# Kernel tuning notes

Measured on AMD Instinct MI355X. Metric: run time of the kernel, lower is better.

## Reference

```python
import jax, jax.numpy as jnp
import numpy as np

B, T, A = 4096, 32, 3
HID, D, N, K = 1024, 128, 16, 4096
FLAT = T * A            # 96
LAT = N * D             # 2048
COMMIT = 0.25


def setup_inputs() -> dict:
    key = jax.random.key(0)
    ks = jax.random.split(key, 14)
    s = 0.02
    return {
        "actions": jax.random.normal(ks[0], (B, T, A), jnp.float32),
        # encoder: FLAT -> HID -> HID -> N*D
        "e_w1": jax.random.normal(ks[1], (FLAT, HID), jnp.float32) * s,
        "e_b1": jnp.zeros((HID,), jnp.float32),
        "e_w2": jax.random.normal(ks[2], (HID, HID), jnp.float32) * s,
        "e_b2": jnp.zeros((HID,), jnp.float32),
        "e_w3": jax.random.normal(ks[3], (HID, LAT), jnp.float32) * s,
        "e_b3": jnp.zeros((LAT,), jnp.float32),
        # codebook init: uniform(-1/K, 1/K) as in torch init
        "codebook": jax.random.uniform(ks[4], (K, D), jnp.float32, -1.0 / K, 1.0 / K),
        # decoder: N*D -> HID -> HID -> FLAT
        "d_w1": jax.random.normal(ks[5], (LAT, HID), jnp.float32) * s,
        "d_b1": jnp.zeros((HID,), jnp.float32),
        "d_w2": jax.random.normal(ks[6], (HID, HID), jnp.float32) * s,
        "d_b2": jnp.zeros((HID,), jnp.float32),
        "d_w3": jax.random.normal(ks[7], (HID, FLAT), jnp.float32) * s,
        "d_b3": jnp.zeros((FLAT,), jnp.float32),
    }


def reference(actions, e_w1, e_b1, e_w2, e_b2, e_w3, e_b3, codebook,
              d_w1, d_b1, d_w2, d_b2, d_w3, d_b3):
    sg = jax.lax.stop_gradient
    b = actions.shape[0]
    # encode: [B, T*A] -> [B, N, D]
    flat = actions.reshape(b, FLAT)
    h = jax.nn.silu(flat @ e_w1 + e_b1)
    h = jax.nn.silu(h @ e_w2 + e_b2)
    latents = (h @ e_w3 + e_b3).reshape(b, N, D)
    # nearest-code search: [B*N, K] squared distances
    fl = latents.reshape(b * N, D)
    dist = (fl * fl).sum(1, keepdims=True) + (codebook * codebook).sum(1)[None, :] - 2.0 * (fl @ codebook.T)
    indices = jnp.argmin(dist, axis=1).reshape(b, N)
    quantized = codebook[indices]                      # [B, N, D]
    codebook_loss = jnp.mean((quantized - sg(latents)) ** 2)
    commitment_loss = jnp.mean((latents - sg(quantized)) ** 2)
    vq_loss = codebook_loss + COMMIT * commitment_loss
    q_st = latents + sg(quantized - latents)           # straight-through
    # decode
    g = jax.nn.silu(q_st.reshape(b, LAT) @ d_w1 + d_b1)
    g = jax.nn.silu(g @ d_w2 + d_b2)
    recon = (g @ d_w3 + d_b3).reshape(b, T, A)
    recon_loss = jnp.mean((recon - actions) ** 2)
    loss = recon_loss + vq_loss
    return recon, indices, vq_loss, recon_loss, loss
```

## Files before the change

kernel.cpp:

```cpp
#include <hip/hip_runtime.h>
#include <hip/hip_bf16.h>

#define DD 128

typedef float f2v __attribute__((ext_vector_type(2)));

__global__ void plant_diag(float val, float* out) {
    if (threadIdx.x == 0 && blockIdx.x == 0) out[0] = val;
}

__global__ void zero_acc(double* acc) {
    if (threadIdx.x == 0 && blockIdx.x == 0) { acc[0] = 0.0; acc[1] = 0.0; }
}

__device__ __forceinline__ float silu_np(float x) {
    float e = (float)exp(-(double)x);
    float u = 1.0f + e;
    float v = 1.0f / u;
    return x * v;
}

template <bool SILU>
__global__ __launch_bounds__(256) void gemm_db(const float* __restrict__ A,
                                               const float* __restrict__ W,
                                               const float* __restrict__ bias,
                                               float* __restrict__ C,
                                               int M, int N, int K) {
    __shared__ __align__(16) float As[128][36];
    __shared__ __align__(16) float Ws[32][68];
    const int t = threadIdx.x;
    const int tx = t & 15, ty = t >> 4;
    const int bm = blockIdx.y * 128, bn = blockIdx.x * 64;

    float acc[8][4];
#pragma unroll
    for (int i = 0; i < 8; ++i)
#pragma unroll
        for (int j = 0; j < 4; ++j) acc[i][j] = 0.0f;

    const int nPanels = (K + 31) / 32;
    float ra[16], rw[8];

    {
        const int k0 = 0;
#pragma unroll
        for (int it = 0; it < 16; ++it) {
            int e = t + 256 * it;
            int m = e >> 5, kk = e & 31;
            int mm = bm + m; if (mm >= M) mm = M - 1;
            int kc = k0 + kk;
            ra[it] = (kc < K) ? A[(size_t)mm * K + kc] : 0.0f;
        }
#pragma unroll
        for (int it = 0; it < 8; ++it) {
            int e = t + 256 * it;
            int r = e >> 6, c = e & 63;
            int n = bn + c;
            int kr = k0 + r;
            rw[it] = (kr < K && n < N) ? W[(size_t)kr * N + n] : 0.0f;
        }
    }

    for (int p = 0; p < nPanels; ++p) {
        __syncthreads();
#pragma unroll
        for (int it = 0; it < 16; ++it) {
            int e = t + 256 * it;
            As[e >> 5][e & 31] = ra[it];
        }
#pragma unroll
        for (int it = 0; it < 8; ++it) {
            int e = t + 256 * it;
            Ws[e >> 6][e & 63] = rw[it];
        }
        __syncthreads();

        if (p + 1 < nPanels) {
            const int k0 = (p + 1) * 32;
#pragma unroll
            for (int it = 0; it < 16; ++it) {
                int e = t + 256 * it;
                int m = e >> 5, kk = e & 31;
                int mm = bm + m; if (mm >= M) mm = M - 1;
                int kc = k0 + kk;
                ra[it] = (kc < K) ? A[(size_t)mm * K + kc] : 0.0f;
            }
#pragma unroll
            for (int it = 0; it < 8; ++it) {
                int e = t + 256 * it;
                int r = e >> 6, c = e & 63;
                int n = bn + c;
                int kr = k0 + r;
                rw[it] = (kr < K && n < N) ? W[(size_t)kr * N + n] : 0.0f;
            }
        }

#pragma unroll
        for (int kq = 0; kq < 8; ++kq) {
            float4 a4[8], w4[4];
#pragma unroll
            for (int i = 0; i < 8; ++i)
                a4[i] = *(const float4*)&As[ty + 16 * i][4 * kq];
#pragma unroll
            for (int q = 0; q < 4; ++q)
                w4[q] = *(const float4*)&Ws[4 * kq + q][4 * tx];
#pragma unroll
            for (int q = 0; q < 4; ++q) {
                const float wv[4] = {w4[q].x, w4[q].y, w4[q].z, w4[q].w};
#pragma unroll
                for (int i = 0; i < 8; ++i) {
                    const float av = ((const float*)&a4[i])[q];
#pragma unroll
                    for (int j = 0; j < 4; ++j)
                        acc[i][j] = fmaf(av, wv[j], acc[i][j]);
                }
            }
        }
    }

#pragma unroll
    for (int i = 0; i < 8; ++i) {
        int m = bm + ty + 16 * i;
#pragma unroll
        for (int j = 0; j < 4; ++j) {
            int n = bn + 4 * tx + j;
            if (m < M && n < N) {
                float x = acc[i][j] + bias[n];
                if (SILU) x = silu_np(x);
                C[(size_t)m * N + n] = x;
            }
        }
    }
}

template <bool SILU>
__global__ __launch_bounds__(256) void gemm64(const float* __restrict__ A,
                                              const float* __restrict__ W,
                                              const float* __restrict__ bias,
                                              float* __restrict__ C,
                                              int M, int N, int K) {
    __shared__ __align__(16) float As[64][36];
    __shared__ __align__(16) float Ws[32][68];
    const int t = threadIdx.x;
    const int tx = t & 15, ty = t >> 4;
    const int bm = blockIdx.y * 64, bn = blockIdx.x * 64;

    float acc[4][4];
#pragma unroll
    for (int i = 0; i < 4; ++i)
#pragma unroll
        for (int j = 0; j < 4; ++j) acc[i][j] = 0.0f;

    const int nPanels = (K + 31) / 32;
    float ra[8], rw[8];

    {
        const int k0 = 0;
#pragma unroll
        for (int it = 0; it < 8; ++it) {
            int e = t + 256 * it;
            int m = e >> 5, kk = e & 31;
            int mm = bm + m; if (mm >= M) mm = M - 1;
            int kc = k0 + kk;
            ra[it] = (kc < K) ? A[(size_t)mm * K + kc] : 0.0f;
            int r = e >> 6, c = e & 63;
            int n = bn + c;
            int kr = k0 + r;
            rw[it] = (kr < K && n < N) ? W[(size_t)kr * N + n] : 0.0f;
        }
    }

    for (int p = 0; p < nPanels; ++p) {
        __syncthreads();
#pragma unroll
        for (int it = 0; it < 8; ++it) {
            int e = t + 256 * it;
            As[e >> 5][e & 31] = ra[it];
            Ws[e >> 6][e & 63] = rw[it];
        }
        __syncthreads();

        if (p + 1 < nPanels) {
            const int k0 = (p + 1) * 32;
#pragma unroll
            for (int it = 0; it < 8; ++it) {
                int e = t + 256 * it;
                int m = e >> 5, kk = e & 31;
                int mm = bm + m; if (mm >= M) mm = M - 1;
                int kc = k0 + kk;
                ra[it] = (kc < K) ? A[(size_t)mm * K + kc] : 0.0f;
                int r = e >> 6, c = e & 63;
                int n = bn + c;
                int kr = k0 + r;
                rw[it] = (kr < K && n < N) ? W[(size_t)kr * N + n] : 0.0f;
            }
        }

#pragma unroll
        for (int kq = 0; kq < 8; ++kq) {
            float4 a4[4], w4[4];
#pragma unroll
            for (int i = 0; i < 4; ++i)
                a4[i] = *(const float4*)&As[4 * ty + i][4 * kq];
#pragma unroll
            for (int q = 0; q < 4; ++q)
                w4[q] = *(const float4*)&Ws[4 * kq + q][4 * tx];
#pragma unroll
            for (int q = 0; q < 4; ++q) {
                const float wv[4] = {w4[q].x, w4[q].y, w4[q].z, w4[q].w};
                const float av[4] = {((const float*)&a4[0])[q], ((const float*)&a4[1])[q],
                                     ((const float*)&a4[2])[q], ((const float*)&a4[3])[q]};
#pragma unroll
                for (int i = 0; i < 4; ++i)
#pragma unroll
                    for (int j = 0; j < 4; ++j)
                        acc[i][j] = fmaf(av[i], wv[j], acc[i][j]);
            }
        }
    }

#pragma unroll
    for (int i = 0; i < 4; ++i) {
        int m = bm + 4 * ty + i;
#pragma unroll
        for (int j = 0; j < 4; ++j) {
            int n = bn + 4 * tx + j;
            if (m < M && n < N) {
                float x = acc[i][j] + bias[n];
                if (SILU) x = silu_np(x);
                C[(size_t)m * N + n] = x;
            }
        }
    }
}

__device__ __forceinline__ float pairwise128_sq(const float* __restrict__ x, int stride) {
    float r0 = x[0*stride]*x[0*stride], r1 = x[1*stride]*x[1*stride],
          r2 = x[2*stride]*x[2*stride], r3 = x[3*stride]*x[3*stride],
          r4 = x[4*stride]*x[4*stride], r5 = x[5*stride]*x[5*stride],
          r6 = x[6*stride]*x[6*stride], r7 = x[7*stride]*x[7*stride];
    for (int i = 8; i < 128; i += 8) {
        r0 += x[(i+0)*stride]*x[(i+0)*stride];
        r1 += x[(i+1)*stride]*x[(i+1)*stride];
        r2 += x[(i+2)*stride]*x[(i+2)*stride];
        r3 += x[(i+3)*stride]*x[(i+3)*stride];
        r4 += x[(i+4)*stride]*x[(i+4)*stride];
        r5 += x[(i+5)*stride]*x[(i+5)*stride];
        r6 += x[(i+6)*stride]*x[(i+6)*stride];
        r7 += x[(i+7)*stride]*x[(i+7)*stride];
    }
    return ((r0 + r1) + (r2 + r3)) + ((r4 + r5) + (r6 + r7));
}

__global__ void code_t2(const float* __restrict__ cb, float* __restrict__ t2, int K) {
    int k = blockIdx.x * 256 + threadIdx.x;
    if (k >= K) return;
    t2[k] = pairwise128_sq(cb + (size_t)k * DD, 1);
}

__global__ void cb_pack(const float* __restrict__ cb, float* __restrict__ cbP, int total) {
    int gid = blockIdx.x * 256 + threadIdx.x;
    if (gid >= total) return;
    int pair = gid >> 8;
    int r = gid & 255;
    int d = r >> 1, w = r & 1;
    cbP[gid] = cb[(size_t)(2 * pair + w) * DD + d];
}

#define VQG_ROWS 128
#define VQG_CPP  256
#define VQG_LT   132

__global__ __launch_bounds__(512) void vq_g88p(const float* __restrict__ lat,
                                               const float* __restrict__ cbP,
                                               const float* __restrict__ t2,
                                               float* __restrict__ pbv,
                                               int* __restrict__ pbk,
                                               int K, int rows_total) {
    __shared__ __align__(16) float Ls[VQG_ROWS][VQG_LT];
    __shared__ float T1s[VQG_ROWS];
    __shared__ float bwv[8][VQG_ROWS];
    __shared__ int   bwk[8][VQG_ROWS];

    const int t = threadIdx.x;
    const int tx = t & 15, ty = t >> 4;
    const int wave = t >> 6, lane = t & 63;
    const int r0 = blockIdx.x * VQG_ROWS;

#pragma unroll
    for (int it = 0; it < 8; ++it) {
        int g = t + 512 * it;
        int r = g >> 5, dq = g & 31;
        int rr = r0 + r; if (rr >= rows_total) rr = rows_total - 1;
        const float4 lv = *(const float4*)(lat + (size_t)rr * DD + 4 * dq);
        *(float4*)&Ls[r][4 * dq] = lv;
    }
    __syncthreads();

    if (t < VQG_ROWS) {
        const float* xr = &Ls[t][0];
        float4 q0 = *(const float4*)&xr[0];
        float4 q1 = *(const float4*)&xr[4];
        float a0 = q0.x*q0.x, a1 = q0.y*q0.y, a2 = q0.z*q0.z, a3 = q0.w*q0.w;
        float a4 = q1.x*q1.x, a5 = q1.y*q1.y, a6 = q1.z*q1.z, a7 = q1.w*q1.w;
#pragma unroll
        for (int i = 1; i < 16; ++i) {
            q0 = *(const float4*)&xr[8 * i];
            q1 = *(const float4*)&xr[8 * i + 4];
            a0 += q0.x*q0.x; a1 += q0.y*q0.y; a2 += q0.z*q0.z; a3 += q0.w*q0.w;
            a4 += q1.x*q1.x; a5 += q1.y*q1.y; a6 += q1.z*q1.z; a7 += q1.w*q1.w;
        }
        T1s[t] = ((a0 + a1) + (a2 + a3)) + ((a4 + a5) + (a6 + a7));
    }
    __syncthreads();

    float t1r[8];
#pragma unroll
    for (int i = 0; i < 8; ++i) t1r[i] = T1s[tx + 16 * i];

    float bestv[8]; int bestk[8];
#pragma unroll
    for (int i = 0; i < 8; ++i) { bestv[i] = 3.4e38f; bestk[i] = 0; }

    const int NP = K / VQG_CPP;
#pragma unroll 1
    for (int p = 0; p < NP; ++p) {
        const int kp = p * VQG_CPP;
        const int cbase = kp + 8 * ty;
        const float* cp0 = cbP + (size_t)cbase * DD;
        float t2v[8];
#pragma unroll
        for (int j = 0; j < 8; ++j) t2v[j] = t2[cbase + j];

        f2v s2[8][4];
#pragma unroll
        for (int i = 0; i < 8; ++i)
#pragma unroll
            for (int m = 0; m < 4; ++m) s2[i][m] = (f2v)(0.0f);

#pragma unroll 4
        for (int dq = 0; dq < 32; ++dq) {
            float4 u0[4], u1[4];
#pragma unroll
            for (int m = 0; m < 4; ++m) {
                u0[m] = *(const float4*)(cp0 + m * 256 + 8 * dq);
                u1[m] = *(const float4*)(cp0 + m * 256 + 8 * dq + 4);
            }
#pragma unroll
            for (int i = 0; i < 8; ++i) {
                const float4 la = *(const float4*)&Ls[tx + 16 * i][4 * dq];
                const f2v lx = {la.x, la.x}, ly = {la.y, la.y};
                const f2v lz = {la.z, la.z}, lw = {la.w, la.w};
#pragma unroll
                for (int m = 0; m < 4; ++m) {
                    const f2v c0 = {u0[m].x, u0[m].y};
                    const f2v c1 = {u0[m].z, u0[m].w};
                    const f2v c2 = {u1[m].x, u1[m].y};
                    const f2v c3 = {u1[m].z, u1[m].w};
                    s2[i][m] = __builtin_elementwise_fma(lx, c0, s2[i][m]);
                    s2[i][m] = __builtin_elementwise_fma(ly, c1, s2[i][m]);
                    s2[i][m] = __builtin_elementwise_fma(lz, c2, s2[i][m]);
                    s2[i][m] = __builtin_elementwise_fma(lw, c3, s2[i][m]);
                }
            }
        }

#pragma unroll
        for (int i = 0; i < 8; ++i) {
            const float tt1 = t1r[i];
#pragma unroll
            for (int m = 0; m < 4; ++m) {
                const int c0 = cbase + 2 * m;
                const float d0 = (tt1 + t2v[2 * m + 0]) - 2.0f * s2[i][m].x;
                const float d1 = (tt1 + t2v[2 * m + 1]) - 2.0f * s2[i][m].y;
                if (d0 < bestv[i]) { bestv[i] = d0; bestk[i] = c0; }
                if (d1 < bestv[i]) { bestv[i] = d1; bestk[i] = c0 + 1; }
            }
        }
    }

#pragma unroll
    for (int off = 16; off <= 32; off <<= 1) {
#pragma unroll
        for (int i = 0; i < 8; ++i) {
            float vv = __shfl_xor(bestv[i], off);
            int kk = __shfl_xor(bestk[i], off);
            if (vv < bestv[i] || (vv == bestv[i] && kk < bestk[i])) {
                bestv[i] = vv; bestk[i] = kk;
            }
        }
    }
    if (lane < 16) {
#pragma unroll
        for (int i = 0; i < 8; ++i) {
            bwv[wave][tx + 16 * i] = bestv[i];
            bwk[wave][tx + 16 * i] = bestk[i];
        }
    }
    __syncthreads();
    if (t < VQG_ROWS) {
        float bv = bwv[0][t]; int bk = bwk[0][t];
#pragma unroll
        for (int w = 1; w < 8; ++w) {
            float v = bwv[w][t]; int k = bwk[w][t];
            if (v < bv || (v == bv && k < bk)) { bv = v; bk = k; }
        }
        if (r0 + t < rows_total) {
            pbv[r0 + t] = bv;
            pbk[r0 + t] = bk;
        }
    }
}

__global__ __launch_bounds__(512) void vq_np4(const float* __restrict__ lat,
                                              const float* __restrict__ cb,
                                              const float* __restrict__ t2,
                                              float* __restrict__ pbv,
                                              int* __restrict__ pbk,
                                              int K, int Kc, int rows_total) {
    __shared__ __align__(16) float Ls[128][68];
    __shared__ __align__(16) float Cs[128][68];
    __shared__ float T1s[64];
    __shared__ float T2s[64];
    __shared__ float bwv[8][68];
    __shared__ int   bwk[8][68];

    const int t = threadIdx.x;
    const int tx = t & 15, ty = t >> 4;
    const int wave = t >> 6, lane = t & 63;
    const int r0 = blockIdx.x * 64;
    const int kbeg = blockIdx.y * Kc;
    const int kend = kbeg + Kc;

#pragma unroll
    for (int it = 0; it < 4; ++it) {
        int g = t + 512 * it;
        int row = g >> 5, dq = g & 31;
        int rr = r0 + row; if (rr >= rows_total) rr = rows_total - 1;
        const float4 v = *(const float4*)(lat + (size_t)rr * DD + 4 * dq);
        Ls[4*dq+0][row] = v.x; Ls[4*dq+1][row] = v.y;
        Ls[4*dq+2][row] = v.z; Ls[4*dq+3][row] = v.w;
    }
    __syncthreads();
    if (t < 64) T1s[t] = pairwise128_sq(&Ls[0][t], 68);

    float bestv[4]; int bestk[4];
#pragma unroll
    for (int r = 0; r < 4; ++r) { bestv[r] = 3.4e38f; bestk[r] = 0; }

    float4 pc[4];
    float pt2 = 0.0f;
#pragma unroll
    for (int it = 0; it < 4; ++it) {
        int g = t + 512 * it;
        int c = g >> 5, dq = g & 31;
        int cc = kbeg + c; if (cc >= K) cc = K - 1;
        pc[it] = *(const float4*)(cb + (size_t)cc * DD + 4 * dq);
    }
    if (t < 64) { int cc = kbeg + t; if (cc >= K) cc = K - 1; pt2 = t2[cc]; }

    for (int k0 = kbeg; k0 < kend; k0 += 64) {
        __syncthreads();
#pragma unroll
        for (int it = 0; it < 4; ++it) {
            int g = t + 512 * it;
            int c = g >> 5, dq = g & 31;
            Cs[4*dq+0][c] = pc[it].x; Cs[4*dq+1][c] = pc[it].y;
            Cs[4*dq+2][c] = pc[it].z; Cs[4*dq+3][c] = pc[it].w;
        }
        if (t < 64) T2s[t] = pt2;
        __syncthreads();

        if (k0 + 64 < kend) {
            const int kn = k0 + 64;
#pragma unroll
            for (int it = 0; it < 4; ++it) {
                int g = t + 512 * it;
                int c = g >> 5, dq = g & 31;
                int cc = kn + c; if (cc >= K) cc = K - 1;
                pc[it] = *(const float4*)(cb + (size_t)cc * DD + 4 * dq);
            }
            if (t < 64) { int cc = kn + t; if (cc >= K) cc = K - 1; pt2 = t2[cc]; }
        }

        float s[4][2];
#pragma unroll
        for (int r = 0; r < 4; ++r) { s[r][0] = 0.0f; s[r][1] = 0.0f; }

#pragma unroll 8
        for (int d = 0; d < 128; ++d) {
            const float4 a4 = *(const float4*)&Ls[d][4 * tx];
            const float2 c2 = *(const float2*)&Cs[d][2 * ty];
            const float av[4] = {a4.x, a4.y, a4.z, a4.w};
#pragma unroll
            for (int r = 0; r < 4; ++r) {
                s[r][0] = fmaf(av[r], c2.x, s[r][0]);
                s[r][1] = fmaf(av[r], c2.y, s[r][1]);
            }
        }

#pragma unroll
        for (int r = 0; r < 4; ++r) {
            const float t1 = T1s[4 * tx + r];
#pragma unroll
            for (int j = 0; j < 2; ++j) {
                int kc = k0 + 2 * ty + j;
                float dist = (t1 + T2s[2 * ty + j]) - 2.0f * s[r][j];
                if (kc < K && dist < bestv[r]) { bestv[r] = dist; bestk[r] = kc; }
            }
        }
    }

#pragma unroll
    for (int off = 16; off <= 32; off <<= 1) {
#pragma unroll
        for (int r = 0; r < 4; ++r) {
            float vv = __shfl_xor(bestv[r], off);
            int kk = __shfl_xor(bestk[r], off);
            if (vv < bestv[r] || (vv == bestv[r] && kk < bestk[r])) {
                bestv[r] = vv; bestk[r] = kk;
            }
        }
    }
    if (lane < 16) {
#pragma unroll
        for (int r = 0; r < 4; ++r) {
            bwv[wave][4 * lane + r] = bestv[r];
            bwk[wave][4 * lane + r] = bestk[r];
        }
    }
    __syncthreads();
    if (t < 64) {
        float bv = bwv[0][t]; int bk = bwk[0][t];
#pragma unroll
        for (int w = 1; w < 8; ++w) {
            float v = bwv[w][t]; int k = bwk[w][t];
            if (v < bv || (v == bv && k < bk)) { bv = v; bk = k; }
        }
        if (r0 + t < rows_total) {
            size_t o = (size_t)blockIdx.y * rows_total + (r0 + t);
            pbv[o] = bv;
            pbk[o] = bk;
        }
    }
}

__global__ __launch_bounds__(256) void vq_combine(const float* __restrict__ pbv,
                                                  const int* __restrict__ pbk,
                                                  int S, int rows,
                                                  int* __restrict__ indices,
                                                  double* __restrict__ acc) {
    int r = blockIdx.x * 256 + threadIdx.x;
    float bv = 3.4e38f; int bk = 0;
    if (r < rows) {
        for (int s = 0; s < S; ++s) {
            float v = pbv[(size_t)s * rows + r];
            int k = pbk[(size_t)s * rows + r];
            if (v < bv) { bv = v; bk = k; }
        }
        indices[r] = bk;
    }
    __shared__ double red[256];
    red[threadIdx.x] = (r < rows) ? (double)bv : 0.0;
    __syncthreads();
    for (int s = 128; s > 0; s >>= 1) {
        if (threadIdx.x < s) red[threadIdx.x] += red[threadIdx.x + s];
        __syncthreads();
    }
    if (threadIdx.x == 0) atomicAdd(acc, red[0]);
}

__global__ void q_gather(const int* __restrict__ idx, const float* __restrict__ cb,
                         float* __restrict__ Q, int count, int nlat) {
    int gid = blockIdx.x * 256 + threadIdx.x;
    if (gid >= count) return;
    int m = gid >> 11;
    int j = gid & 2047;
    int code = idx[m * nlat + (j >> 7)];
    Q[gid] = cb[((size_t)code << 7) + (j & 127)];
}

__global__ __launch_bounds__(256) void recon_out(const float* __restrict__ recon,
                                                 const float* __restrict__ actions,
                                                 float* __restrict__ out,
                                                 double* __restrict__ acc, int count) {
    int gid = blockIdx.x * 256 + threadIdx.x;
    double sq = 0.0;
    if (gid < count) {
        float rv = recon[gid];
        float av = actions[gid];
        double diff = (double)rv - (double)av;
        out[gid] = rv;
        sq = diff * diff;
    }
    __shared__ double red[256];
    red[threadIdx.x] = sq;
    __syncthreads();
    for (int s = 128; s > 0; s >>= 1) {
        if (threadIdx.x < s) red[threadIdx.x] += red[threadIdx.x + s];
        __syncthreads();
    }
    if (threadIdx.x == 0) atomicAdd(acc + 1, red[0]);
}

__global__ void idx_out(const int* __restrict__ idx, float* __restrict__ out, int count) {
    int gid = blockIdx.x * 256 + threadIdx.x;
    if (gid < count) out[gid] = (float)idx[gid];
}

__global__ void finalize(const double* __restrict__ acc, float* __restrict__ out,
                         double vq_den, double rec_den) {
    double vq = 1.25 * acc[0] / vq_den;
    double rl = acc[1] / rec_den;
    out[0] = (float)vq;
    out[1] = (float)rl;
    out[2] = (float)(rl + vq);
}

static inline int ceildiv(int a, int b) { return (a + b - 1) / b; }

extern "C" void kernel_launch(void* const* d_in, const int* in_sizes, int n_in,
                              void* d_out, int out_size, void* d_ws, size_t ws_size,
                              hipStream_t stream) {
    const float* actions = (const float*)d_in[0];
    const float* e_w1 = (const float*)d_in[1];
    const float* e_b1 = (const float*)d_in[2];
    const float* e_w2 = (const float*)d_in[3];
    const float* e_b2 = (const float*)d_in[4];
    const float* e_w3 = (const float*)d_in[5];
    const float* e_b3 = (const float*)d_in[6];
    const float* cb   = (const float*)d_in[7];
    const float* d_w1 = (const float*)d_in[8];
    const float* d_b1 = (const float*)d_in[9];
    const float* d_w2 = (const float*)d_in[10];
    const float* d_b2 = (const float*)d_in[11];
    const float* d_w3 = (const float*)d_in[12];
    const float* d_b3 = (const float*)d_in[13];
    float* out = (float*)d_out;

    const int FLAT = in_sizes[13];
    const int B    = in_sizes[0] / FLAT;
    const int HID  = in_sizes[2];
    const int LAT  = in_sizes[6];
    const int K    = in_sizes[7] / DD;
    const int NL   = LAT / DD;

    const bool g88 = (K % VQG_CPP == 0);
    const int S = 1;
    const int Kc = K;

    int CHUNK = B;
    auto need = [&](int ch) -> size_t {
        return (size_t)ch * HID * 4 * 2 + (size_t)ch * LAT * 4 * 2
             + (size_t)ch * HID * 4 * 2 + (size_t)ch * FLAT * 4
             + (size_t)K * 4 + (size_t)K * DD * 4 + 64 + (size_t)B * NL * 4
             + (size_t)ch * NL * S * 8;
    };
    while (CHUNK > 16 && need(CHUNK) > ws_size) CHUNK >>= 1;
    if (need(CHUNK) > ws_size) {
        plant_diag<<<1, 64, 0, stream>>>(2222.0f, out);
        return;
    }
    const int NCHUNK = ceildiv(B, CHUNK);

    char* ws = (char*)d_ws;
    size_t off = 0;
    float* h1c  = (float*)(ws + off); off += (size_t)CHUNK * HID * 4;
    float* h2c  = (float*)(ws + off); off += (size_t)CHUNK * HID * 4;
    float* latc = (float*)(ws + off); off += (size_t)CHUNK * LAT * 4;
    float* Qc   = (float*)(ws + off); off += (size_t)CHUNK * LAT * 4;
    float* g1c  = (float*)(ws + off); off += (size_t)CHUNK * HID * 4;
    float* g2c  = (float*)(ws + off); off += (size_t)CHUNK * HID * 4;
    float* recc = (float*)(ws + off); off += (size_t)CHUNK * FLAT * 4;
    float* t2   = (float*)(ws + off); off += (size_t)K * 4;
    float* cbP  = (float*)(ws + off); off += (size_t)K * DD * 4;
    double* acc = (double*)(ws + off); off += 64;
    int*   idx  = (int*)(ws + off);   off += (size_t)B * NL * 4;
    float* pbv  = (float*)(ws + off); off += (size_t)CHUNK * NL * S * 4;
    int*   pbk  = (int*)(ws + off);

    zero_acc<<<1, 64, 0, stream>>>(acc);
    code_t2<<<ceildiv(K, 256), 256, 0, stream>>>(cb, t2, K);
    if (g88) {
        cb_pack<<<ceildiv(K * DD, 256), 256, 0, stream>>>(cb, cbP, K * DD);
    }

    auto GEMM = [&](bool silu, const float* Araw, const float* Wt, const float* bias,
                    float* Cout, int M, int N, int Kd) {
        if (N < 128) {
            dim3 grid(ceildiv(N, 64), ceildiv(M, 64));
            if (silu) gemm64<true><<<grid, 256, 0, stream>>>(Araw, Wt, bias, Cout, M, N, Kd);
            else      gemm64<false><<<grid, 256, 0, stream>>>(Araw, Wt, bias, Cout, M, N, Kd);
        } else {
            dim3 grid(ceildiv(N, 64), ceildiv(M, 128));
            if (silu) gemm_db<true><<<grid, 256, 0, stream>>>(Araw, Wt, bias, Cout, M, N, Kd);
            else      gemm_db<false><<<grid, 256, 0, stream>>>(Araw, Wt, bias, Cout, M, N, Kd);
        }
    };

    for (int c = 0; c < NCHUNK; ++c) {
        const int r0 = c * CHUNK;
        const int cbR = (B - r0 < CHUNK) ? (B - r0) : CHUNK;
        const float* act_c = actions + (size_t)r0 * FLAT;
        int* idx_c = idx + (size_t)r0 * NL;
        const int rows = cbR * NL;

        GEMM(true,  act_c, e_w1, e_b1, h1c, cbR, HID, FLAT);
        GEMM(true,  h1c,   e_w2, e_b2, h2c, cbR, HID, HID);
        GEMM(false, h2c,   e_w3, e_b3, latc, cbR, LAT, HID);

        if (g88) {
            vq_g88p<<<ceildiv(rows, VQG_ROWS), 512, 0, stream>>>(
                latc, cbP, t2, pbv, pbk, K, rows);
        } else {
            vq_np4<<<dim3(ceildiv(rows, 64), S), 512, 0, stream>>>(
                latc, cb, t2, pbv, pbk, K, Kc, rows);
        }
        vq_combine<<<ceildiv(rows, 256), 256, 0, stream>>>(pbv, pbk, S, rows, idx_c, acc);

        q_gather<<<ceildiv(cbR * LAT, 256), 256, 0, stream>>>(idx_c, cb, Qc, cbR * LAT, NL);
        GEMM(true,  Qc,  d_w1, d_b1, g1c, cbR, HID, LAT);
        GEMM(true,  g1c, d_w2, d_b2, g2c, cbR, HID, HID);
        GEMM(false, g2c, d_w3, d_b3, recc, cbR, FLAT, HID);

        recon_out<<<ceildiv(cbR * FLAT, 256), 256, 0, stream>>>(
            recc, act_c, out + (size_t)r0 * FLAT, acc, cbR * FLAT);
    }

    idx_out<<<ceildiv(B * NL, 256), 256, 0, stream>>>(idx, out + (size_t)B * FLAT, B * NL);
    finalize<<<1, 1, 0, stream>>>(acc, out + (size_t)B * FLAT + (size_t)B * NL,
                                  (double)B * NL * DD, (double)B * FLAT);
}
```

Measured before the change: 1.806 ms.

## Widen FP32 GEMM tile to 128x128 with 8x8 per-thread outputs

Replaces the 128x64 double-buffered GEMM with a 128x128 tile where each thread computes an 8x8 block, which raises arithmetic intensity per shared-memory load. The W panel is no longer register-prefetched; it is loaded straight into shared memory inside the loop after the barrier, so only the A panel stays double-buffered. Epilogue stores become float4 vectorized. This trades fewer blocks and more accumulator registers, with possible occupancy loss, for better data reuse. W load latency is now exposed rather than overlapped with compute.

```diff
diff --git a/kernel.cpp b/kernel.cpp
--- a/kernel.cpp
+++ b/kernel.cpp
@@ -21,25 +21,25 @@
 }
 
 template <bool SILU>
-__global__ __launch_bounds__(256) void gemm_db(const float* __restrict__ A,
-                                               const float* __restrict__ W,
-                                               const float* __restrict__ bias,
-                                               float* __restrict__ C,
-                                               int M, int N, int K) {
+__global__ __launch_bounds__(256) void gemm88(const float* __restrict__ A,
+                                              const float* __restrict__ W,
+                                              const float* __restrict__ bias,
+                                              float* __restrict__ C,
+                                              int M, int N, int K) {
     __shared__ __align__(16) float As[128][36];
-    __shared__ __align__(16) float Ws[32][68];
+    __shared__ __align__(16) float Ws[32][132];
     const int t = threadIdx.x;
     const int tx = t & 15, ty = t >> 4;
-    const int bm = blockIdx.y * 128, bn = blockIdx.x * 64;
-
-    float acc[8][4];
+    const int bm = blockIdx.y * 128, bn = blockIdx.x * 128;
+
+    float acc[8][8];
 #pragma unroll
     for (int i = 0; i < 8; ++i)
 #pragma unroll
-        for (int j = 0; j < 4; ++j) acc[i][j] = 0.0f;
+        for (int j = 0; j < 8; ++j) acc[i][j] = 0.0f;
 
     const int nPanels = (K + 31) / 32;
-    float ra[16], rw[8];
+    float ra[16];
 
     {
         const int k0 = 0;
@@ -51,14 +51,6 @@
             int kc = k0 + kk;
             ra[it] = (kc < K) ? A[(size_t)mm * K + kc] : 0.0f;
         }
-#pragma unroll
-        for (int it = 0; it < 8; ++it) {
-            int e = t + 256 * it;
-            int r = e >> 6, c = e & 63;
-            int n = bn + c;
-            int kr = k0 + r;
-            rw[it] = (kr < K && n < N) ? W[(size_t)kr * N + n] : 0.0f;
-        }
     }
 
     for (int p = 0; p < nPanels; ++p) {
@@ -68,10 +60,17 @@
             int e = t + 256 * it;
             As[e >> 5][e & 31] = ra[it];
         }
-#pragma unroll
-        for (int it = 0; it < 8; ++it) {
-            int e = t + 256 * it;
-            Ws[e >> 6][e & 63] = rw[it];
+        {
+            const int kp0 = 32 * p;
+#pragma unroll
+            for (int it = 0; it < 16; ++it) {
+                int e = t + 256 * it;
+                int r = e >> 7, c = e & 127;
+                int n = bn + c;
+                int kr = kp0 + r;
+                float wv = (kr < K && n < N) ? W[(size_t)kr * N + n] : 0.0f;
+                Ws[r][c] = wv;
+            }
         }
         __syncthreads();
 
@@ -85,34 +84,32 @@
                 int kc = k0 + kk;
                 ra[it] = (kc < K) ? A[(size_t)mm * K + kc] : 0.0f;
             }
-#pragma unroll
-            for (int it = 0; it < 8; ++it) {
-                int e = t + 256 * it;
-                int r = e >> 6, c = e & 63;
-                int n = bn + c;
-                int kr = k0 + r;
-                rw[it] = (kr < K && n < N) ? W[(size_t)kr * N + n] : 0.0f;
-            }
         }
 
 #pragma unroll
         for (int kq = 0; kq < 8; ++kq) {
-            float4 a4[8], w4[4];
+            float4 a4[8], wA[4], wB[4];
 #pragma unroll
             for (int i = 0; i < 8; ++i)
                 a4[i] = *(const float4*)&As[ty + 16 * i][4 * kq];
 #pragma unroll
-            for (int q = 0; q < 4; ++q)
-                w4[q] = *(const float4*)&Ws[4 * kq + q][4 * tx];
-#pragma unroll
             for (int q = 0; q < 4; ++q) {
-                const float wv[4] = {w4[q].x, w4[q].y, w4[q].z, w4[q].w};
+                wA[q] = *(const float4*)&Ws[4 * kq + q][4 * tx];
+                wB[q] = *(const float4*)&Ws[4 * kq + q][64 + 4 * tx];
+            }
+#pragma unroll
+            for (int q = 0; q < 4; ++q) {
+                const float w0[4] = {wA[q].x, wA[q].y, wA[q].z, wA[q].w};
+                const float w1[4] = {wB[q].x, wB[q].y, wB[q].z, wB[q].w};
 #pragma unroll
                 for (int i = 0; i < 8; ++i) {
                     const float av = ((const float*)&a4[i])[q];
 #pragma unroll
                     for (int j = 0; j < 4; ++j)
-                        acc[i][j] = fmaf(av, wv[j], acc[i][j]);
+                        acc[i][j] = fmaf(av, w0[j], acc[i][j]);
+#pragma unroll
+                    for (int j = 0; j < 4; ++j)
+                        acc[i][4 + j] = fmaf(av, w1[j], acc[i][4 + j]);
                 }
             }
         }
@@ -121,13 +118,51 @@
 #pragma unroll
     for (int i = 0; i < 8; ++i) {
         int m = bm + ty + 16 * i;
-#pragma unroll
-        for (int j = 0; j < 4; ++j) {
-            int n = bn + 4 * tx + j;
-            if (m < M && n < N) {
-                float x = acc[i][j] + bias[n];
-                if (SILU) x = silu_np(x);
-                C[(size_t)m * N + n] = x;
+        if (m >= M) continue;
+        {
+            int n0 = bn + 4 * tx;
+            if (n0 + 3 < N) {
+                float4 o;
+                float x0 = acc[i][0] + bias[n0 + 0];
+                float x1 = acc[i][1] + bias[n0 + 1];
+                float x2 = acc[i][2] + bias[n0 + 2];
+                float x3 = acc[i][3] + bias[n0 + 3];
+                if (SILU) { x0 = silu_np(x0); x1 = silu_np(x1); x2 = silu_np(x2); x3 = silu_np(x3); }
+                o.x = x0; o.y = x1; o.z = x2; o.w = x3;
+                *(float4*)&C[(size_t)m * N + n0] = o;
+            } else {
+#pragma unroll
+                for (int j = 0; j < 4; ++j) {
+                    int n = n0 + j;
+                    if (n < N) {
+                        float x = acc[i][j] + bias[n];
+                        if (SILU) x = silu_np(x);
+                        C[(size_t)m * N + n] = x;
+                    }
+                }
+            }
+        }
+        {
+            int n1 = bn + 64 + 4 * tx;
+            if (n1 + 3 < N) {
+                float4 o;
+                float x0 = acc[i][4] + bias[n1 + 0];
+                float x1 = acc[i][5] + bias[n1 + 1];
+                float x2 = acc[i][6] + bias[n1 + 2];
+                float x3 = acc[i][7] + bias[n1 + 3];
+                if (SILU) { x0 = silu_np(x0); x1 = silu_np(x1); x2 = silu_np(x2); x3 = silu_np(x3); }
+                o.x = x0; o.y = x1; o.z = x2; o.w = x3;
+                *(float4*)&C[(size_t)m * N + n1] = o;
+            } else {
+#pragma unroll
+                for (int j = 0; j < 4; ++j) {
+                    int n = n1 + j;
+                    if (n < N) {
+                        float x = acc[i][4 + j] + bias[n];
+                        if (SILU) x = silu_np(x);
+                        C[(size_t)m * N + n] = x;
+                    }
+                }
             }
         }
     }
@@ -692,9 +727,9 @@
             if (silu) gemm64<true><<<grid, 256, 0, stream>>>(Araw, Wt, bias, Cout, M, N, Kd);
             else      gemm64<false><<<grid, 256, 0, stream>>>(Araw, Wt, bias, Cout, M, N, Kd);
         } else {
-            dim3 grid(ceildiv(N, 64), ceildiv(M, 128));
-            if (silu) gemm_db<true><<<grid, 256, 0, stream>>>(Araw, Wt, bias, Cout, M, N, Kd);
-            else      gemm_db<false><<<grid, 256, 0, stream>>>(Araw, Wt, bias, Cout, M, N, Kd);
+            dim3 grid(ceildiv(N, 128), ceildiv(M, 128));
+            if (silu) gemm88<true><<<grid, 256, 0, stream>>>(Araw, Wt, bias, Cout, M, N, Kd);
+            else      gemm88<false><<<grid, 256, 0, stream>>>(Araw, Wt, bias, Cout, M, N, Kd);
         }
     };
 
```

Result: slower. 2.714 ms (+50.3%).
